# Kernel optimization log

Measured on AMD Instinct MI355X. Metric: run time of the kernel, lower is better.

## Reference

```python
import jax, jax.numpy as jnp
import numpy as np

HIDDEN = 1024
FFN = 2048
N_EXPERTS = 8
TOP_K = 2


def setup_inputs() -> dict:
    key = jax.random.key(0)
    k_x, k_g, k1, k2, k3 = jax.random.split(key, 5)
    hidden_states = jax.random.normal(k_x, (4, 4096, HIDDEN), dtype=jnp.float32)
    gate_w = jax.random.normal(k_g, (N_EXPERTS, HIDDEN), dtype=jnp.float32) * 0.02
    # nn.Linear convention: weight is [out_features, in_features]
    w1 = jax.random.normal(k1, (N_EXPERTS, FFN, HIDDEN), dtype=jnp.float32) * 0.02
    w2 = jax.random.normal(k2, (N_EXPERTS, HIDDEN, FFN), dtype=jnp.float32) * 0.02
    w3 = jax.random.normal(k3, (N_EXPERTS, FFN, HIDDEN), dtype=jnp.float32) * 0.02
    return {"hidden_states": hidden_states, "gate_w": gate_w, "w1": w1, "w2": w2, "w3": w3}


def reference(hidden_states, gate_w, w1, w2, w3):
    B, S, H = hidden_states.shape
    E = gate_w.shape[0]
    x = hidden_states.reshape(-1, H)  # [T, H]
    T = x.shape[0]

    # Router: softmax in fp32, top-2, renormalize (matches torch reference)
    router_logits = jnp.einsum("th,eh->te", x, gate_w)
    probs = jax.nn.softmax(router_logits.astype(jnp.float32), axis=-1)
    top_w, top_i = jax.lax.top_k(probs, TOP_K)  # [T, 2]
    top_w = top_w / jnp.sum(top_w, axis=-1, keepdims=True)
    top_w = top_w.astype(x.dtype)

    # Dense combine weights [T, E]: zero for unselected experts.
    combine = jnp.zeros((T, E), dtype=x.dtype)
    combine = combine.at[jnp.arange(T)[:, None], top_i].set(top_w)

    # Per-expert SwiGLU; loop over small fixed expert count, accumulate.
    out = jnp.zeros_like(x)
    for e in range(E):
        h = jax.nn.silu(x @ w1[e].T) * (x @ w3[e].T)  # [T, FFN]
        out = out + combine[:, e:e + 1] * (h @ w2[e].T)
    return out.reshape(B, S, H)
```

## Files before the change

### kernel.cpp

```cpp
#include <hip/hip_runtime.h>
#include <cstdint>

#define H 1024
#define F 2048
#define E_N 8
#define BM 128
#define BK 64

typedef __attribute__((ext_vector_type(8))) short short8v;
typedef __attribute__((ext_vector_type(4))) float float4v;
typedef unsigned short u16;

__device__ __forceinline__ u16 f2bf(float f) {
    uint32_t u = __float_as_uint(f);
    u += 0x7FFFu + ((u >> 16) & 1u);
    return (u16)(u >> 16);
}
__device__ __forceinline__ float bf2f(u16 b) {
    return __uint_as_float(((uint32_t)b) << 16);
}

__device__ __forceinline__ void gload16(const void* g, void* l) {
    __builtin_amdgcn_global_load_lds((const __attribute__((address_space(1))) uint32_t*)g,
                                     (__attribute__((address_space(3))) uint32_t*)l, 16, 0, 0);
}

__device__ __forceinline__ void decode_swz(int bid, int nTiles, int ngy, int gyc,
                                           int& tile, int& gy) {
    int nblk = nTiles * ngy;
    int q = nblk >> 3, r = nblk & 7;
    int xcd = bid & 7, pos = bid >> 3;
    int cid = (xcd < r ? xcd * (q + 1) : r * (q + 1) + (xcd - r) * q) + pos;
    int per = nTiles * gyc;
    int chunk = cid / per, rem = cid - chunk * per;
    tile = rem / gyc;
    gy = chunk * gyc + (rem - (rem / gyc) * gyc);
}

__global__ __launch_bounds__(256) void cvt_kernel(const float* __restrict__ src,
                                                  u16* __restrict__ dst, int n) {
    int i = (blockIdx.x * 256 + threadIdx.x) * 4;
    int stride = gridDim.x * 256 * 4;
    for (; i < n; i += stride) {
        float4 v = *(const float4*)(src + i);
        ushort4 o;
        o.x = f2bf(v.x); o.y = f2bf(v.y); o.z = f2bf(v.z); o.w = f2bf(v.w);
        *(ushort4*)(dst + i) = o;
    }
}

__global__ __launch_bounds__(256) void router_kernel(const float* __restrict__ x,
                                                     const float* __restrict__ gw,
                                                     int* __restrict__ topi,
                                                     float* __restrict__ topw, int T) {
    int wave = threadIdx.x >> 6, lane = threadIdx.x & 63;
    int t = blockIdx.x * 4 + wave;
    if (t >= T) return;
    const float4* xr = (const float4*)(x + (size_t)t * H);
    float4 xv[4];
#pragma unroll
    for (int i = 0; i < 4; i++) xv[i] = xr[i * 64 + lane];
    float acc[E_N];
#pragma unroll
    for (int e = 0; e < E_N; e++) {
        const float4* gr = (const float4*)(gw + e * H);
        float s = 0.f;
#pragma unroll
        for (int i = 0; i < 4; i++) {
            float4 g = gr[i * 64 + lane];
            s += xv[i].x * g.x + xv[i].y * g.y + xv[i].z * g.z + xv[i].w * g.w;
        }
        acc[e] = s;
    }
#pragma unroll
    for (int e = 0; e < E_N; e++) {
#pragma unroll
        for (int off = 32; off; off >>= 1) acc[e] += __shfl_xor(acc[e], off, 64);
    }
    if (lane == 0) {
        int i0 = 0;
#pragma unroll
        for (int e = 1; e < E_N; e++) if (acc[e] > acc[i0]) i0 = e;
        int i1 = -1;
#pragma unroll
        for (int e = 0; e < E_N; e++) {
            if (e == i0) continue;
            if (i1 < 0 || acc[e] > acc[i1]) i1 = e;
        }
        float e1 = __expf(acc[i1] - acc[i0]);
        float w0 = 1.f / (1.f + e1);
        float w1v = e1 / (1.f + e1);
        topi[t * 2] = i0; topi[t * 2 + 1] = i1;
        topw[t * 2] = w0; topw[t * 2 + 1] = w1v;
    }
}

__global__ __launch_bounds__(256) void hist_kernel(const int* __restrict__ topi,
                                                   int* __restrict__ counts, int n) {
    __shared__ int hc[E_N];
    if (threadIdx.x < E_N) hc[threadIdx.x] = 0;
    __syncthreads();
    for (int i = blockIdx.x * 256 + threadIdx.x; i < n; i += gridDim.x * 256)
        atomicAdd(&hc[topi[i]], 1);
    __syncthreads();
    if (threadIdx.x < E_N) atomicAdd(&counts[threadIdx.x], hc[threadIdx.x]);
}

__global__ void scan_kernel(const int* __restrict__ counts, int* __restrict__ offsets,
                            int* __restrict__ cursors, int* __restrict__ tileOff) {
    if (threadIdx.x == 0 && blockIdx.x == 0) {
        int o = 0, to = 0;
        for (int e = 0; e < E_N; e++) {
            offsets[e] = o; cursors[e] = o; tileOff[e] = to;
            o += counts[e];
            to += (counts[e] + BM - 1) / BM;
        }
        offsets[E_N] = o; tileOff[E_N] = to;
    }
}

__global__ __launch_bounds__(1024) void scatter_kernel(const int* __restrict__ topi,
                                                       const float* __restrict__ topw,
                                                       int* __restrict__ cursors,
                                                       int* __restrict__ perm_tok,
                                                       float* __restrict__ perm_gate,
                                                       int* __restrict__ inv, int n) {
    __shared__ int hc[E_N];
    __shared__ int base[E_N];
    int tid = threadIdx.x;
    if (tid < E_N) hc[tid] = 0;
    __syncthreads();
    int i = blockIdx.x * 1024 + tid;
    int e = 0, lrank = 0;
    bool ok = (i < n);
    if (ok) {
        e = topi[i];
        lrank = atomicAdd(&hc[e], 1);
    }
    __syncthreads();
    if (tid < E_N) base[tid] = atomicAdd(&cursors[tid], hc[tid]);
    __syncthreads();
    if (ok) {
        int pos = base[e] + lrank;
        perm_tok[pos] = i >> 1;
        perm_gate[pos] = topw[i];
        inv[i] = pos;
    }
}

__global__ __launch_bounds__(256) void stage1_kernel(
    const u16* __restrict__ xg, const u16* __restrict__ w1b, const u16* __restrict__ w3b,
    const int* __restrict__ perm_tok, const float* __restrict__ perm_gate,
    const int* __restrict__ offsets, const int* __restrict__ tileOff,
    u16* __restrict__ h, int cstart, int tpcThis) {
    __shared__ u16 lA[BM * BK];
    __shared__ u16 lB1[64 * BK];
    __shared__ u16 lB3[64 * BK];
    __shared__ int ptokS[BM];
    __shared__ float pgateS[BM];

    int tileL, nbIdx;
    decode_swz(blockIdx.x, tpcThis, F / 64, 4, tileL, nbIdx);
    int tile = cstart + tileL;
    if (tile >= tileOff[E_N]) return;
    int e = 0;
    while (e < E_N - 1 && tile >= tileOff[e + 1]) e++;
    int rbase = offsets[e] + (tile - tileOff[e]) * BM;
    int segEnd = offsets[e + 1];
    int e0 = 0;
    while (e0 < E_N - 1 && cstart >= tileOff[e0 + 1]) e0++;
    int chunkBase = offsets[e0] + (cstart - tileOff[e0]) * BM;

    int tid = threadIdx.x;
    if (tid < BM) {
        int p = rbase + tid; if (p > segEnd - 1) p = segEnd - 1;
        ptokS[tid] = perm_tok[p];
        pgateS[tid] = perm_gate[p];
    }
    __syncthreads();

    int lane = tid & 63, wave = tid >> 6;
    int mBase = (wave >> 1) * 64, nBaseW = (wave & 1) * 32;
    int lrow = lane & 15, kgrp = lane >> 4;
    int nb = nbIdx * 64;
    const u16* w1p = w1b + (size_t)e * F * H + (size_t)nb * H;
    const u16* w3p = w3b + (size_t)e * F * H + (size_t)nb * H;

    int lr = lane >> 3;
    int csw = ((lane & 7) ^ lr) << 3;

    const u16* aSrc[4];
#pragma unroll
    for (int j = 0; j < 4; j++) {
        int rb = (j * 4 + wave) * 8;
        int tok = ptokS[rb + lr];
        aSrc[j] = xg + (size_t)tok * H + csw;
    }
    const u16 *b1Src[2], *b3Src[2];
#pragma unroll
    for (int j = 0; j < 2; j++) {
        int rr = (j * 4 + wave) * 8 + lr;
        b1Src[j] = w1p + (size_t)rr * H + csw;
        b3Src[j] = w3p + (size_t)rr * H + csw;
    }

    float4v acc1[4][2], acc3[4][2];
#pragma unroll
    for (int a = 0; a < 4; a++)
#pragma unroll
        for (int b = 0; b < 2; b++) { acc1[a][b] = (float4v)(0.f); acc3[a][b] = (float4v)(0.f); }

    for (int kt = 0; kt < H / BK; kt++) {
        int ko = kt * BK;
#pragma unroll
        for (int j = 0; j < 4; j++)
            gload16(aSrc[j] + ko, &lA[((j * 4 + wave) * 8) * BK]);
#pragma unroll
        for (int j = 0; j < 2; j++) {
            int rb = (j * 4 + wave) * 8;
            gload16(b1Src[j] + ko, &lB1[rb * BK]);
            gload16(b3Src[j] + ko, &lB3[rb * BK]);
        }
        __syncthreads();
#pragma unroll
        for (int kk = 0; kk < 2; kk++) {
            int kg = kk * 4 + kgrp;
            short8v aF[4], b1F[2], b3F[2];
#pragma unroll
            for (int fm = 0; fm < 4; fm++) {
                int r = mBase + fm * 16 + lrow;
                aF[fm] = *(const short8v*)&lA[r * BK + ((kg ^ (r & 7)) << 3)];
            }
#pragma unroll
            for (int fn = 0; fn < 2; fn++) {
                int c = nBaseW + fn * 16 + lrow;
                b1F[fn] = *(const short8v*)&lB1[c * BK + ((kg ^ (c & 7)) << 3)];
                b3F[fn] = *(const short8v*)&lB3[c * BK + ((kg ^ (c & 7)) << 3)];
            }
#pragma unroll
            for (int fm = 0; fm < 4; fm++)
#pragma unroll
                for (int fn = 0; fn < 2; fn++) {
                    acc1[fm][fn] = __builtin_amdgcn_mfma_f32_16x16x32_bf16(aF[fm], b1F[fn], acc1[fm][fn], 0, 0, 0);
                    acc3[fm][fn] = __builtin_amdgcn_mfma_f32_16x16x32_bf16(aF[fm], b3F[fn], acc3[fm][fn], 0, 0, 0);
                }
        }
        __syncthreads();
    }
    int rif = (lane >> 4) * 4;
#pragma unroll
    for (int fm = 0; fm < 4; fm++) {
#pragma unroll
        for (int reg = 0; reg < 4; reg++) {
            int rowIdx = mBase + fm * 16 + rif + reg;
            int p = rbase + rowIdx;
            if (p < segEnd) {
                float g = pgateS[rowIdx];
#pragma unroll
                for (int fn = 0; fn < 2; fn++) {
                    float a1 = acc1[fm][fn][reg], a3 = acc3[fm][fn][reg];
                    float sv = a1 / (1.f + __expf(-a1));
                    float hv = sv * a3 * g;
                    int ncol = nb + nBaseW + fn * 16 + (lane & 15);
                    h[(size_t)(p - chunkBase) * F + ncol] = f2bf(hv);
                }
            }
        }
    }
}

__global__ __launch_bounds__(256) void stage2_kernel(
    const u16* __restrict__ h, const u16* __restrict__ w2b,
    const int* __restrict__ offsets, const int* __restrict__ tileOff,
    u16* __restrict__ y, int cstart, int tpcThis) {
    __shared__ u16 lA[BM * BK];
    __shared__ u16 lB[BM * BK];

    int tileL, nbIdx;
    decode_swz(blockIdx.x, tpcThis, H / 128, 4, tileL, nbIdx);
    int tile = cstart + tileL;
    if (tile >= tileOff[E_N]) return;
    int e = 0;
    while (e < E_N - 1 && tile >= tileOff[e + 1]) e++;
    int rbase = offsets[e] + (tile - tileOff[e]) * BM;
    int segEnd = offsets[e + 1];
    int e0 = 0;
    while (e0 < E_N - 1 && cstart >= tileOff[e0 + 1]) e0++;
    int chunkBase = offsets[e0] + (cstart - tileOff[e0]) * BM;

    int tid = threadIdx.x;
    int lane = tid & 63, wave = tid >> 6;
    int mBase = (wave >> 1) * 64, nBaseW = (wave & 1) * 64;
    int lrow = lane & 15, kgrp = lane >> 4;
    int nb = nbIdx * 128;
    const u16* w2p = w2b + (size_t)e * H * F + (size_t)nb * F;

    int lr = lane >> 3;
    int csw = ((lane & 7) ^ lr) << 3;

    const u16 *aSrc[4], *bSrc[4];
#pragma unroll
    for (int j = 0; j < 4; j++) {
        int rb = (j * 4 + wave) * 8;
        int p = rbase + rb + lr; if (p > segEnd - 1) p = segEnd - 1;
        aSrc[j] = h + (size_t)(p - chunkBase) * F + csw;
        int rr = rb + lr;
        bSrc[j] = w2p + (size_t)rr * F + csw;
    }

    float4v acc[4][4];
#pragma unroll
    for (int a = 0; a < 4; a++)
#pragma unroll
        for (int b = 0; b < 4; b++) acc[a][b] = (float4v)(0.f);

    for (int kt = 0; kt < F / BK; kt++) {
        int ko = kt * BK;
#pragma unroll
        for (int j = 0; j < 4; j++) {
            int rb = (j * 4 + wave) * 8;
            gload16(aSrc[j] + ko, &lA[rb * BK]);
            gload16(bSrc[j] + ko, &lB[rb * BK]);
        }
        __syncthreads();
#pragma unroll
        for (int kk = 0; kk < 2; kk++) {
            int kg = kk * 4 + kgrp;
            short8v aF[4], bF[4];
#pragma unroll
            for (int fm = 0; fm < 4; fm++) {
                int r = mBase + fm * 16 + lrow;
                aF[fm] = *(const short8v*)&lA[r * BK + ((kg ^ (r & 7)) << 3)];
            }
#pragma unroll
            for (int fn = 0; fn < 4; fn++) {
                int c = nBaseW + fn * 16 + lrow;
                bF[fn] = *(const short8v*)&lB[c * BK + ((kg ^ (c & 7)) << 3)];
            }
#pragma unroll
            for (int fm = 0; fm < 4; fm++)
#pragma unroll
                for (int fn = 0; fn < 4; fn++)
                    acc[fm][fn] = __builtin_amdgcn_mfma_f32_16x16x32_bf16(aF[fm], bF[fn], acc[fm][fn], 0, 0, 0);
        }
        __syncthreads();
    }
    int rif = (lane >> 4) * 4;
#pragma unroll
    for (int fm = 0; fm < 4; fm++) {
#pragma unroll
        for (int reg = 0; reg < 4; reg++) {
            int rowIdx = mBase + fm * 16 + rif + reg;
            int p = rbase + rowIdx;
            if (p < segEnd) {
#pragma unroll
                for (int fn = 0; fn < 4; fn++) {
                    int n = nb + nBaseW + fn * 16 + (lane & 15);
                    y[(size_t)p * H + n] = f2bf(acc[fm][fn][reg]);
                }
            }
        }
    }
}

__global__ __launch_bounds__(256) void combine_kernel(const u16* __restrict__ y,
                                                      const int* __restrict__ inv,
                                                      float* __restrict__ out) {
    int t = blockIdx.x, c = threadIdx.x;
    int s0 = inv[t * 2], s1 = inv[t * 2 + 1];
    ushort4 a = *(const ushort4*)(y + (size_t)s0 * H + c * 4);
    ushort4 b = *(const ushort4*)(y + (size_t)s1 * H + c * 4);
    float4 o;
    o.x = bf2f(a.x) + bf2f(b.x);
    o.y = bf2f(a.y) + bf2f(b.y);
    o.z = bf2f(a.z) + bf2f(b.z);
    o.w = bf2f(a.w) + bf2f(b.w);
    *(float4*)(out + (size_t)t * H + c * 4) = o;
}

extern "C" void kernel_launch(void* const* d_in, const int* in_sizes, int n_in,
                              void* d_out, int out_size, void* d_ws, size_t ws_size,
                              hipStream_t stream) {
    (void)n_in; (void)out_size;
    const float* x  = (const float*)d_in[0];
    const float* gw = (const float*)d_in[1];
    const float* w1 = (const float*)d_in[2];
    const float* w2 = (const float*)d_in[3];
    const float* w3 = (const float*)d_in[4];
    float* out = (float*)d_out;
    int T = in_sizes[0] / H;
    int P = T * 2;

    char* ws = (char*)d_ws;
    size_t off = 0;
    auto alloc = [&](size_t b) { size_t c = off; off = (off + b + 255) & ~(size_t)255; return c; };
    size_t misc_o  = alloc(256);
    int* counts  = (int*)(ws + misc_o);
    int* offsets = (int*)(ws + misc_o + 64);
    int* cursors = (int*)(ws + misc_o + 128);
    int* tileOff = (int*)(ws + misc_o + 192);
    size_t topi_o  = alloc((size_t)T * 2 * 4);
    size_t topw_o  = alloc((size_t)T * 2 * 4);
    size_t ptok_o  = alloc((size_t)P * 4);
    size_t pgate_o = alloc((size_t)P * 4);
    size_t inv_o   = alloc((size_t)T * 2 * 4);
    size_t w1b_o = alloc((size_t)E_N * F * H * 2);
    size_t w3b_o = alloc((size_t)E_N * F * H * 2);
    size_t w2b_o = alloc((size_t)E_N * H * F * 2);
    size_t xg_o  = alloc((size_t)T * H * 2);
    size_t y_o   = alloc((size_t)P * H * 2);

    int maxTiles = P / BM + E_N;
    size_t perTile = (size_t)BM * F * 2;
    size_t avail = (ws_size > off + 256) ? (ws_size - off - 256) : 0;
    int tpc = (int)(avail / perTile);
    if (tpc > maxTiles) tpc = maxTiles;
    if (tpc < 8) tpc = 8;
    size_t h_o = alloc((size_t)tpc * perTile);

    hipMemsetAsync(ws + misc_o, 0, 256, stream);

    int nW = E_N * F * H;
    cvt_kernel<<<4096, 256, 0, stream>>>(w1, (u16*)(ws + w1b_o), nW);
    cvt_kernel<<<4096, 256, 0, stream>>>(w3, (u16*)(ws + w3b_o), nW);
    cvt_kernel<<<4096, 256, 0, stream>>>(w2, (u16*)(ws + w2b_o), nW);
    cvt_kernel<<<4096, 256, 0, stream>>>(x,  (u16*)(ws + xg_o),  T * H);

    router_kernel<<<T / 4, 256, 0, stream>>>(x, gw, (int*)(ws + topi_o), (float*)(ws + topw_o), T);
    hist_kernel<<<32, 256, 0, stream>>>((int*)(ws + topi_o), counts, P);
    scan_kernel<<<1, 64, 0, stream>>>(counts, offsets, cursors, tileOff);
    scatter_kernel<<<(P + 1023) / 1024, 1024, 0, stream>>>(
        (int*)(ws + topi_o), (float*)(ws + topw_o), cursors,
        (int*)(ws + ptok_o), (float*)(ws + pgate_o), (int*)(ws + inv_o), P);

    for (int cstart = 0; cstart < maxTiles; cstart += tpc) {
        int tpcThis = maxTiles - cstart; if (tpcThis > tpc) tpcThis = tpc;
        stage1_kernel<<<tpcThis * (F / 64), 256, 0, stream>>>(
            (u16*)(ws + xg_o), (u16*)(ws + w1b_o), (u16*)(ws + w3b_o),
            (int*)(ws + ptok_o), (float*)(ws + pgate_o), offsets, tileOff,
            (u16*)(ws + h_o), cstart, tpcThis);
        stage2_kernel<<<tpcThis * (H / 128), 256, 0, stream>>>(
            (u16*)(ws + h_o), (u16*)(ws + w2b_o), offsets, tileOff,
            (u16*)(ws + y_o), cstart, tpcThis);
    }
    combine_kernel<<<T, 256, 0, stream>>>((u16*)(ws + y_o), (int*)(ws + inv_o), out);
}
```

Measured before the change: 752.6 us.

## Double-buffer LDS tiles in both expert GEMM stages to overlap loads with MFMA

Both grouped-GEMM kernels now use two LDS buffers per operand and prefetch the next K-tile with global_load_lds while MFMAs run on the current tile. An explicit vmcnt(0) wait plus one barrier per iteration replaces the old load-then-sync-then-compute pattern. The aim is to hide global memory latency behind compute. In exchange, LDS use per block doubles, which may reduce occupancy.

```diff
diff --git a/kernel.cpp b/kernel.cpp
--- a/kernel.cpp
+++ b/kernel.cpp
@@ -153,9 +153,9 @@
     const int* __restrict__ perm_tok, const float* __restrict__ perm_gate,
     const int* __restrict__ offsets, const int* __restrict__ tileOff,
     u16* __restrict__ h, int cstart, int tpcThis) {
-    __shared__ u16 lA[BM * BK];
-    __shared__ u16 lB1[64 * BK];
-    __shared__ u16 lB3[64 * BK];
+    __shared__ u16 lA[2][BM * BK];
+    __shared__ u16 lB1[2][64 * BK];
+    __shared__ u16 lB3[2][64 * BK];
     __shared__ int ptokS[BM];
     __shared__ float pgateS[BM];
 
@@ -204,24 +204,32 @@
         b3Src[j] = w3p + (size_t)rr * H + csw;
     }
 
-    float4v acc1[4][2], acc3[4][2];
-#pragma unroll
-    for (int a = 0; a < 4; a++)
-#pragma unroll
-        for (int b = 0; b < 2; b++) { acc1[a][b] = (float4v)(0.f); acc3[a][b] = (float4v)(0.f); }
-
-    for (int kt = 0; kt < H / BK; kt++) {
+    auto stage = [&](int kt, int b) {
         int ko = kt * BK;
 #pragma unroll
         for (int j = 0; j < 4; j++)
-            gload16(aSrc[j] + ko, &lA[((j * 4 + wave) * 8) * BK]);
+            gload16(aSrc[j] + ko, &lA[b][((j * 4 + wave) * 8) * BK]);
 #pragma unroll
         for (int j = 0; j < 2; j++) {
             int rb = (j * 4 + wave) * 8;
-            gload16(b1Src[j] + ko, &lB1[rb * BK]);
-            gload16(b3Src[j] + ko, &lB3[rb * BK]);
-        }
-        __syncthreads();
+            gload16(b1Src[j] + ko, &lB1[b][rb * BK]);
+            gload16(b3Src[j] + ko, &lB3[b][rb * BK]);
+        }
+    };
+
+    float4v acc1[4][2], acc3[4][2];
+#pragma unroll
+    for (int a = 0; a < 4; a++)
+#pragma unroll
+        for (int b = 0; b < 2; b++) { acc1[a][b] = (float4v)(0.f); acc3[a][b] = (float4v)(0.f); }
+
+    stage(0, 0);
+    asm volatile("s_waitcnt vmcnt(0)" ::: "memory");
+    __syncthreads();
+
+    for (int kt = 0; kt < H / BK; kt++) {
+        int cur = kt & 1;
+        if (kt + 1 < H / BK) stage(kt + 1, cur ^ 1);
 #pragma unroll
         for (int kk = 0; kk < 2; kk++) {
             int kg = kk * 4 + kgrp;
@@ -229,13 +237,13 @@
 #pragma unroll
             for (int fm = 0; fm < 4; fm++) {
                 int r = mBase + fm * 16 + lrow;
-                aF[fm] = *(const short8v*)&lA[r * BK + ((kg ^ (r & 7)) << 3)];
+                aF[fm] = *(const short8v*)&lA[cur][r * BK + ((kg ^ (r & 7)) << 3)];
             }
 #pragma unroll
             for (int fn = 0; fn < 2; fn++) {
                 int c = nBaseW + fn * 16 + lrow;
-                b1F[fn] = *(const short8v*)&lB1[c * BK + ((kg ^ (c & 7)) << 3)];
-                b3F[fn] = *(const short8v*)&lB3[c * BK + ((kg ^ (c & 7)) << 3)];
+                b1F[fn] = *(const short8v*)&lB1[cur][c * BK + ((kg ^ (c & 7)) << 3)];
+                b3F[fn] = *(const short8v*)&lB3[cur][c * BK + ((kg ^ (c & 7)) << 3)];
             }
 #pragma unroll
             for (int fm = 0; fm < 4; fm++)
@@ -245,6 +253,7 @@
                     acc3[fm][fn] = __builtin_amdgcn_mfma_f32_16x16x32_bf16(aF[fm], b3F[fn], acc3[fm][fn], 0, 0, 0);
                 }
         }
+        asm volatile("s_waitcnt vmcnt(0)" ::: "memory");
         __syncthreads();
     }
     int rif = (lane >> 4) * 4;
@@ -273,8 +282,8 @@
     const u16* __restrict__ h, const u16* __restrict__ w2b,
     const int* __restrict__ offsets, const int* __restrict__ tileOff,
     u16* __restrict__ y, int cstart, int tpcThis) {
-    __shared__ u16 lA[BM * BK];
-    __shared__ u16 lB[BM * BK];
+    __shared__ u16 lA[2][BM * BK];
+    __shared__ u16 lB[2][BM * BK];
 
     int tileL, nbIdx;
     decode_swz(blockIdx.x, tpcThis, H / 128, 4, tileL, nbIdx);
@@ -308,21 +317,29 @@
         bSrc[j] = w2p + (size_t)rr * F + csw;
     }
 
-    float4v acc[4][4];
-#pragma unroll
-    for (int a = 0; a < 4; a++)
-#pragma unroll
-        for (int b = 0; b < 4; b++) acc[a][b] = (float4v)(0.f);
-
-    for (int kt = 0; kt < F / BK; kt++) {
+    auto stage = [&](int kt, int b) {
         int ko = kt * BK;
 #pragma unroll
         for (int j = 0; j < 4; j++) {
             int rb = (j * 4 + wave) * 8;
-            gload16(aSrc[j] + ko, &lA[rb * BK]);
-            gload16(bSrc[j] + ko, &lB[rb * BK]);
-        }
-        __syncthreads();
+            gload16(aSrc[j] + ko, &lA[b][rb * BK]);
+            gload16(bSrc[j] + ko, &lB[b][rb * BK]);
+        }
+    };
+
+    float4v acc[4][4];
+#pragma unroll
+    for (int a = 0; a < 4; a++)
+#pragma unroll
+        for (int b = 0; b < 4; b++) acc[a][b] = (float4v)(0.f);
+
+    stage(0, 0);
+    asm volatile("s_waitcnt vmcnt(0)" ::: "memory");
+    __syncthreads();
+
+    for (int kt = 0; kt < F / BK; kt++) {
+        int cur = kt & 1;
+        if (kt + 1 < F / BK) stage(kt + 1, cur ^ 1);
 #pragma unroll
         for (int kk = 0; kk < 2; kk++) {
             int kg = kk * 4 + kgrp;
@@ -330,12 +347,12 @@
 #pragma unroll
             for (int fm = 0; fm < 4; fm++) {
                 int r = mBase + fm * 16 + lrow;
-                aF[fm] = *(const short8v*)&lA[r * BK + ((kg ^ (r & 7)) << 3)];
+                aF[fm] = *(const short8v*)&lA[cur][r * BK + ((kg ^ (r & 7)) << 3)];
             }
 #pragma unroll
             for (int fn = 0; fn < 4; fn++) {
                 int c = nBaseW + fn * 16 + lrow;
-                bF[fn] = *(const short8v*)&lB[c * BK + ((kg ^ (c & 7)) << 3)];
+                bF[fn] = *(const short8v*)&lB[cur][c * BK + ((kg ^ (c & 7)) << 3)];
             }
 #pragma unroll
             for (int fm = 0; fm < 4; fm++)
@@ -343,6 +360,7 @@
                 for (int fn = 0; fn < 4; fn++)
                     acc[fm][fn] = __builtin_amdgcn_mfma_f32_16x16x32_bf16(aF[fm], bF[fn], acc[fm][fn], 0, 0, 0);
         }
+        asm volatile("s_waitcnt vmcnt(0)" ::: "memory");
         __syncthreads();
     }
     int rif = (lane >> 4) * 4;
```

Measured after the change: 829.8 us. 1.1x slower.

## Double-buffer expert GEMMs with 256-row tiles and interleaved prefetch

Applied to the files above, without the earlier changes.

Both expert GEMM stages now use 256-row tiles with 512-thread blocks and double-buffered LDS. The next K-slice's global-to-LDS loads are interleaved with MFMA phases under explicit vmcnt waits, barriers and setprio. This is meant to hide memory latency and raise arithmetic intensity per block. Stage 2 picks a 256- or 128-wide N tile depending on how many tiles a chunk has. In exchange it uses more registers and LDS per block and wastes more work on partially filled expert tiles.

```diff
diff --git a/kernel.cpp b/kernel.cpp
--- a/kernel.cpp
+++ b/kernel.cpp
@@ -4,7 +4,7 @@
 #define H 1024
 #define F 2048
 #define E_N 8
-#define BM 128
+#define BM 256
 #define BK 64
 
 typedef __attribute__((ext_vector_type(8))) short short8v;
@@ -23,6 +23,12 @@
 __device__ __forceinline__ void gload16(const void* g, void* l) {
     __builtin_amdgcn_global_load_lds((const __attribute__((address_space(1))) uint32_t*)g,
                                      (__attribute__((address_space(3))) uint32_t*)l, 16, 0, 0);
+}
+
+__device__ __forceinline__ void barx() {
+    asm volatile("" ::: "memory");
+    __builtin_amdgcn_s_barrier();
+    asm volatile("" ::: "memory");
 }
 
 __device__ __forceinline__ void decode_swz(int bid, int nTiles, int ngy, int gyc,
@@ -148,19 +154,19 @@
     }
 }
 
-__global__ __launch_bounds__(256) void stage1_kernel(
+__global__ __launch_bounds__(512) void stage1_kernel(
     const u16* __restrict__ xg, const u16* __restrict__ w1b, const u16* __restrict__ w3b,
     const int* __restrict__ perm_tok, const float* __restrict__ perm_gate,
     const int* __restrict__ offsets, const int* __restrict__ tileOff,
     u16* __restrict__ h, int cstart, int tpcThis) {
-    __shared__ u16 lA[BM * BK];
-    __shared__ u16 lB1[64 * BK];
-    __shared__ u16 lB3[64 * BK];
+    __shared__ u16 lA[2][BM * BK];
+    __shared__ u16 lB1[2][128 * BK];
+    __shared__ u16 lB3[2][128 * BK];
     __shared__ int ptokS[BM];
     __shared__ float pgateS[BM];
 
     int tileL, nbIdx;
-    decode_swz(blockIdx.x, tpcThis, F / 64, 4, tileL, nbIdx);
+    decode_swz(blockIdx.x, tpcThis, F / 128, 4, tileL, nbIdx);
     int tile = cstart + tileL;
     if (tile >= tileOff[E_N]) return;
     int e = 0;
@@ -179,89 +185,122 @@
     }
     __syncthreads();
 
-    int lane = tid & 63, wave = tid >> 6;
-    int mBase = (wave >> 1) * 64, nBaseW = (wave & 1) * 32;
+    int lane = tid & 63, wid = tid >> 6;
+    int wr = wid >> 2, wc = wid & 3;
     int lrow = lane & 15, kgrp = lane >> 4;
-    int nb = nbIdx * 64;
+    int lr = lane >> 3, csw = ((lane & 7) ^ lr) << 3;
+    int nb = nbIdx * 128;
     const u16* w1p = w1b + (size_t)e * F * H + (size_t)nb * H;
     const u16* w3p = w3b + (size_t)e * F * H + (size_t)nb * H;
 
-    int lr = lane >> 3;
-    int csw = ((lane & 7) ^ lr) << 3;
-
-    const u16* aSrc[4];
+    int aOff[4];
 #pragma unroll
     for (int j = 0; j < 4; j++) {
-        int rb = (j * 4 + wave) * 8;
-        int tok = ptokS[rb + lr];
-        aSrc[j] = xg + (size_t)tok * H + csw;
-    }
-    const u16 *b1Src[2], *b3Src[2];
-#pragma unroll
-    for (int j = 0; j < 2; j++) {
-        int rr = (j * 4 + wave) * 8 + lr;
-        b1Src[j] = w1p + (size_t)rr * H + csw;
-        b3Src[j] = w3p + (size_t)rr * H + csw;
-    }
-
-    float4v acc1[4][2], acc3[4][2];
-#pragma unroll
-    for (int a = 0; a < 4; a++)
+        int rb = (j * 8 + wid) * 8;
+        aOff[j] = ptokS[rb + lr] * H + csw;
+    }
+    int bOff[2];
+#pragma unroll
+    for (int j = 0; j < 2; j++) bOff[j] = ((j * 8 + wid) * 8 + lr) * H + csw;
+
+    auto stA  = [&](int cc, int ko, int j) { gload16(xg  + aOff[j] + ko, &lA[cc][(j * 8 + wid) * 8 * BK]); };
+    auto stB1 = [&](int cc, int ko, int j) { gload16(w1p + bOff[j] + ko, &lB1[cc][(j * 8 + wid) * 8 * BK]); };
+    auto stB3 = [&](int cc, int ko, int j) { gload16(w3p + bOff[j] + ko, &lB3[cc][(j * 8 + wid) * 8 * BK]); };
+
+    float4v acc1[8][2], acc3[8][2];
+#pragma unroll
+    for (int a = 0; a < 8; a++)
 #pragma unroll
         for (int b = 0; b < 2; b++) { acc1[a][b] = (float4v)(0.f); acc3[a][b] = (float4v)(0.f); }
 
-    for (int kt = 0; kt < H / BK; kt++) {
-        int ko = kt * BK;
-#pragma unroll
-        for (int j = 0; j < 4; j++)
-            gload16(aSrc[j] + ko, &lA[((j * 4 + wave) * 8) * BK]);
-#pragma unroll
-        for (int j = 0; j < 2; j++) {
-            int rb = (j * 4 + wave) * 8;
-            gload16(b1Src[j] + ko, &lB1[rb * BK]);
-            gload16(b3Src[j] + ko, &lB3[rb * BK]);
-        }
-        __syncthreads();
-#pragma unroll
-        for (int kk = 0; kk < 2; kk++) {
-            int kg = kk * 4 + kgrp;
-            short8v aF[4], b1F[2], b3F[2];
-#pragma unroll
-            for (int fm = 0; fm < 4; fm++) {
-                int r = mBase + fm * 16 + lrow;
-                aF[fm] = *(const short8v*)&lA[r * BK + ((kg ^ (r & 7)) << 3)];
+    stB1(0, 0, 0); stB1(0, 0, 1);
+    stB3(0, 0, 0); stB3(0, 0, 1);
+    stA(0, 0, 0);  stA(0, 0, 2);
+    stA(0, 0, 1);  stA(0, 0, 3);
+    asm volatile("s_waitcnt vmcnt(2)" ::: "memory");
+    barx();
+
+#define S1_DS(p) \
+    short8v aF##p[2][2]; \
+    _Pragma("unroll") \
+    for (int pm = 0; pm < 2; pm++) { \
+        int r = wr * 128 + (2 * p + pm) * 16 + lrow; \
+        _Pragma("unroll") \
+        for (int kk = 0; kk < 2; kk++) \
+            aF##p[pm][kk] = *(const short8v*)&Ac[r * BK + (((kk * 4 + kgrp) ^ (r & 7)) << 3)]; \
+    }
+#define S1_MM(p) \
+    __builtin_amdgcn_s_setprio(1); \
+    _Pragma("unroll") \
+    for (int pm = 0; pm < 2; pm++) \
+    _Pragma("unroll") \
+    for (int n = 0; n < 2; n++) \
+    _Pragma("unroll") \
+    for (int kk = 0; kk < 2; kk++) { \
+        acc1[2 * p + pm][n] = __builtin_amdgcn_mfma_f32_16x16x32_bf16(aF##p[pm][kk], b1F[n][kk], acc1[2 * p + pm][n], 0, 0, 0); \
+        acc3[2 * p + pm][n] = __builtin_amdgcn_mfma_f32_16x16x32_bf16(aF##p[pm][kk], b3F[n][kk], acc3[2 * p + pm][n], 0, 0, 0); \
+    } \
+    __builtin_amdgcn_s_setprio(0);
+
+    const int NT = H / BK;
+    for (int t = 0; t < NT; t++) {
+        int c = t & 1, cN = c ^ 1;
+        int ko = (t + 1) * BK;
+        bool pf = (t + 1 < NT);
+        const u16* Ac = lA[c]; const u16* B1c = lB1[c]; const u16* B3c = lB3[c];
+        short8v b1F[2][2], b3F[2][2];
+#pragma unroll
+        for (int n = 0; n < 2; n++) {
+            int col = wc * 32 + n * 16 + lrow;
+#pragma unroll
+            for (int kk = 0; kk < 2; kk++) {
+                int so = col * BK + (((kk * 4 + kgrp) ^ (col & 7)) << 3);
+                b1F[n][kk] = *(const short8v*)&B1c[so];
+                b3F[n][kk] = *(const short8v*)&B3c[so];
             }
-#pragma unroll
-            for (int fn = 0; fn < 2; fn++) {
-                int c = nBaseW + fn * 16 + lrow;
-                b1F[fn] = *(const short8v*)&lB1[c * BK + ((kg ^ (c & 7)) << 3)];
-                b3F[fn] = *(const short8v*)&lB3[c * BK + ((kg ^ (c & 7)) << 3)];
-            }
-#pragma unroll
-            for (int fm = 0; fm < 4; fm++)
-#pragma unroll
-                for (int fn = 0; fn < 2; fn++) {
-                    acc1[fm][fn] = __builtin_amdgcn_mfma_f32_16x16x32_bf16(aF[fm], b1F[fn], acc1[fm][fn], 0, 0, 0);
-                    acc3[fm][fn] = __builtin_amdgcn_mfma_f32_16x16x32_bf16(aF[fm], b3F[fn], acc3[fm][fn], 0, 0, 0);
-                }
-        }
-        __syncthreads();
-    }
+        }
+        S1_DS(0)
+        if (pf) { stB1(cN, ko, 0); stB1(cN, ko, 1); }
+        barx();
+        S1_MM(0)
+        barx();
+        S1_DS(1)
+        if (pf) { stB3(cN, ko, 0); stB3(cN, ko, 1); }
+        barx();
+        S1_MM(1)
+        if (pf) asm volatile("s_waitcnt vmcnt(4)" ::: "memory");
+        else    asm volatile("s_waitcnt vmcnt(0)" ::: "memory");
+        barx();
+        S1_DS(2)
+        if (pf) { stA(cN, ko, 0); stA(cN, ko, 2); }
+        barx();
+        S1_MM(2)
+        barx();
+        S1_DS(3)
+        if (pf) { stA(cN, ko, 1); stA(cN, ko, 3); }
+        barx();
+        S1_MM(3)
+        asm volatile("s_waitcnt vmcnt(2)" ::: "memory");
+        barx();
+    }
+#undef S1_DS
+#undef S1_MM
+
     int rif = (lane >> 4) * 4;
 #pragma unroll
-    for (int fm = 0; fm < 4; fm++) {
+    for (int m = 0; m < 8; m++) {
 #pragma unroll
         for (int reg = 0; reg < 4; reg++) {
-            int rowIdx = mBase + fm * 16 + rif + reg;
+            int rowIdx = wr * 128 + m * 16 + rif + reg;
             int p = rbase + rowIdx;
             if (p < segEnd) {
                 float g = pgateS[rowIdx];
 #pragma unroll
-                for (int fn = 0; fn < 2; fn++) {
-                    float a1 = acc1[fm][fn][reg], a3 = acc3[fm][fn][reg];
+                for (int n = 0; n < 2; n++) {
+                    float a1 = acc1[m][n][reg], a3 = acc3[m][n][reg];
                     float sv = a1 / (1.f + __expf(-a1));
                     float hv = sv * a3 * g;
-                    int ncol = nb + nBaseW + fn * 16 + (lane & 15);
+                    int ncol = nb + wc * 32 + n * 16 + (lane & 15);
                     h[(size_t)(p - chunkBase) * F + ncol] = f2bf(hv);
                 }
             }
@@ -269,15 +308,17 @@
     }
 }
 
-__global__ __launch_bounds__(256) void stage2_kernel(
+template<int NREP>
+__global__ __launch_bounds__(512) void stage2_kernel(
     const u16* __restrict__ h, const u16* __restrict__ w2b,
     const int* __restrict__ offsets, const int* __restrict__ tileOff,
     u16* __restrict__ y, int cstart, int tpcThis) {
-    __shared__ u16 lA[BM * BK];
-    __shared__ u16 lB[BM * BK];
+    constexpr int BN = NREP * 64;
+    __shared__ u16 lA[2][BM * BK];
+    __shared__ u16 lB[2][BN * BK];
 
     int tileL, nbIdx;
-    decode_swz(blockIdx.x, tpcThis, H / 128, 4, tileL, nbIdx);
+    decode_swz(blockIdx.x, tpcThis, H / BN, 4, tileL, nbIdx);
     int tile = cstart + tileL;
     if (tile >= tileOff[E_N]) return;
     int e = 0;
@@ -289,74 +330,120 @@
     int chunkBase = offsets[e0] + (cstart - tileOff[e0]) * BM;
 
     int tid = threadIdx.x;
-    int lane = tid & 63, wave = tid >> 6;
-    int mBase = (wave >> 1) * 64, nBaseW = (wave & 1) * 64;
+    int lane = tid & 63, wid = tid >> 6;
+    int wr = wid >> 2, wc = wid & 3;
     int lrow = lane & 15, kgrp = lane >> 4;
-    int nb = nbIdx * 128;
+    int lr = lane >> 3, csw = ((lane & 7) ^ lr) << 3;
+    int nb = nbIdx * BN;
     const u16* w2p = w2b + (size_t)e * H * F + (size_t)nb * F;
 
-    int lr = lane >> 3;
-    int csw = ((lane & 7) ^ lr) << 3;
-
-    const u16 *aSrc[4], *bSrc[4];
+    int aOff[4];
 #pragma unroll
     for (int j = 0; j < 4; j++) {
-        int rb = (j * 4 + wave) * 8;
+        int rb = (j * 8 + wid) * 8;
         int p = rbase + rb + lr; if (p > segEnd - 1) p = segEnd - 1;
-        aSrc[j] = h + (size_t)(p - chunkBase) * F + csw;
-        int rr = rb + lr;
-        bSrc[j] = w2p + (size_t)rr * F + csw;
-    }
-
-    float4v acc[4][4];
-#pragma unroll
-    for (int a = 0; a < 4; a++)
-#pragma unroll
-        for (int b = 0; b < 4; b++) acc[a][b] = (float4v)(0.f);
-
-    for (int kt = 0; kt < F / BK; kt++) {
-        int ko = kt * BK;
-#pragma unroll
-        for (int j = 0; j < 4; j++) {
-            int rb = (j * 4 + wave) * 8;
-            gload16(aSrc[j] + ko, &lA[rb * BK]);
-            gload16(bSrc[j] + ko, &lB[rb * BK]);
-        }
-        __syncthreads();
-#pragma unroll
-        for (int kk = 0; kk < 2; kk++) {
-            int kg = kk * 4 + kgrp;
-            short8v aF[4], bF[4];
-#pragma unroll
-            for (int fm = 0; fm < 4; fm++) {
-                int r = mBase + fm * 16 + lrow;
-                aF[fm] = *(const short8v*)&lA[r * BK + ((kg ^ (r & 7)) << 3)];
-            }
-#pragma unroll
-            for (int fn = 0; fn < 4; fn++) {
-                int c = nBaseW + fn * 16 + lrow;
-                bF[fn] = *(const short8v*)&lB[c * BK + ((kg ^ (c & 7)) << 3)];
-            }
-#pragma unroll
-            for (int fm = 0; fm < 4; fm++)
-#pragma unroll
-                for (int fn = 0; fn < 4; fn++)
-                    acc[fm][fn] = __builtin_amdgcn_mfma_f32_16x16x32_bf16(aF[fm], bF[fn], acc[fm][fn], 0, 0, 0);
-        }
-        __syncthreads();
-    }
+        aOff[j] = (p - chunkBase) * F + csw;
+    }
+    int bOff[NREP];
+#pragma unroll
+    for (int j = 0; j < NREP; j++) bOff[j] = ((j * 8 + wid) * 8 + lr) * F + csw;
+
+    auto stA = [&](int cc, int ko, int j) { gload16(h   + aOff[j] + ko, &lA[cc][(j * 8 + wid) * 8 * BK]); };
+    auto stB = [&](int cc, int ko, int j) { gload16(w2p + bOff[j] + ko, &lB[cc][(j * 8 + wid) * 8 * BK]); };
+
+    float4v acc[8][NREP];
+#pragma unroll
+    for (int a = 0; a < 8; a++)
+#pragma unroll
+        for (int b = 0; b < NREP; b++) acc[a][b] = (float4v)(0.f);
+
+#pragma unroll
+    for (int j = 0; j < NREP; j++) stB(0, 0, j);
+    stA(0, 0, 0); stA(0, 0, 2);
+    stA(0, 0, 1); stA(0, 0, 3);
+    asm volatile("s_waitcnt vmcnt(2)" ::: "memory");
+    barx();
+
+#define S2_DS(p) \
+    short8v aF##p[2][2]; \
+    _Pragma("unroll") \
+    for (int pm = 0; pm < 2; pm++) { \
+        int r = wr * 128 + (2 * p + pm) * 16 + lrow; \
+        _Pragma("unroll") \
+        for (int kk = 0; kk < 2; kk++) \
+            aF##p[pm][kk] = *(const short8v*)&Ac[r * BK + (((kk * 4 + kgrp) ^ (r & 7)) << 3)]; \
+    }
+#define S2_MM(p) \
+    __builtin_amdgcn_s_setprio(1); \
+    _Pragma("unroll") \
+    for (int pm = 0; pm < 2; pm++) \
+    _Pragma("unroll") \
+    for (int n = 0; n < NREP; n++) \
+    _Pragma("unroll") \
+    for (int kk = 0; kk < 2; kk++) \
+        acc[2 * p + pm][n] = __builtin_amdgcn_mfma_f32_16x16x32_bf16(aF##p[pm][kk], bF[n][kk], acc[2 * p + pm][n], 0, 0, 0); \
+    __builtin_amdgcn_s_setprio(0);
+
+    const int NT = F / BK;
+    for (int t = 0; t < NT; t++) {
+        int c = t & 1, cN = c ^ 1;
+        int ko = (t + 1) * BK;
+        bool pf = (t + 1 < NT);
+        const u16* Ac = lA[c]; const u16* Bc = lB[c];
+        short8v bF[NREP][2];
+#pragma unroll
+        for (int n = 0; n < NREP; n++) {
+            int col = wc * (BN / 4) + n * 16 + lrow;
+#pragma unroll
+            for (int kk = 0; kk < 2; kk++)
+                bF[n][kk] = *(const short8v*)&Bc[col * BK + (((kk * 4 + kgrp) ^ (col & 7)) << 3)];
+        }
+        S2_DS(0)
+        if (pf) { stB(cN, ko, 0); if constexpr (NREP == 4) stB(cN, ko, 1); }
+        barx();
+        S2_MM(0)
+        barx();
+        S2_DS(1)
+        if (pf) {
+            if constexpr (NREP == 4) { stB(cN, ko, 2); stB(cN, ko, 3); }
+            else stB(cN, ko, 1);
+        }
+        barx();
+        S2_MM(1)
+        if (pf) {
+            if constexpr (NREP == 4) asm volatile("s_waitcnt vmcnt(4)" ::: "memory");
+            else                     asm volatile("s_waitcnt vmcnt(2)" ::: "memory");
+        } else {
+            asm volatile("s_waitcnt vmcnt(0)" ::: "memory");
+        }
+        barx();
+        S2_DS(2)
+        if (pf) { stA(cN, ko, 0); stA(cN, ko, 2); }
+        barx();
+        S2_MM(2)
+        barx();
+        S2_DS(3)
+        if (pf) { stA(cN, ko, 1); stA(cN, ko, 3); }
+        barx();
+        S2_MM(3)
+        asm volatile("s_waitcnt vmcnt(2)" ::: "memory");
+        barx();
+    }
+#undef S2_DS
+#undef S2_MM
+
     int rif = (lane >> 4) * 4;
 #pragma unroll
-    for (int fm = 0; fm < 4; fm++) {
+    for (int m = 0; m < 8; m++) {
 #pragma unroll
         for (int reg = 0; reg < 4; reg++) {
-            int rowIdx = mBase + fm * 16 + rif + reg;
+            int rowIdx = wr * 128 + m * 16 + rif + reg;
             int p = rbase + rowIdx;
             if (p < segEnd) {
 #pragma unroll
-                for (int fn = 0; fn < 4; fn++) {
-                    int n = nb + nBaseW + fn * 16 + (lane & 15);
-                    y[(size_t)p * H + n] = f2bf(acc[fm][fn][reg]);
+                for (int n = 0; n < NREP; n++) {
+                    int col = nb + wc * (BN / 4) + n * 16 + (lane & 15);
+                    y[(size_t)p * H + col] = f2bf(acc[m][n][reg]);
                 }
             }
         }
@@ -415,7 +502,7 @@
     size_t avail = (ws_size > off + 256) ? (ws_size - off - 256) : 0;
     int tpc = (int)(avail / perTile);
     if (tpc > maxTiles) tpc = maxTiles;
-    if (tpc < 8) tpc = 8;
+    if (tpc < 4) tpc = 4;
     size_t h_o = alloc((size_t)tpc * perTile);
 
     hipMemsetAsync(ws + misc_o, 0, 256, stream);
@@ -435,13 +522,18 @@
 
     for (int cstart = 0; cstart < maxTiles; cstart += tpc) {
         int tpcThis = maxTiles - cstart; if (tpcThis > tpc) tpcThis = tpc;
-        stage1_kernel<<<tpcThis * (F / 64), 256, 0, stream>>>(
+        stage1_kernel<<<tpcThis * (F / 128), 512, 0, stream>>>(
             (u16*)(ws + xg_o), (u16*)(ws + w1b_o), (u16*)(ws + w3b_o),
             (int*)(ws + ptok_o), (float*)(ws + pgate_o), offsets, tileOff,
             (u16*)(ws + h_o), cstart, tpcThis);
-        stage2_kernel<<<tpcThis * (H / 128), 256, 0, stream>>>(
-            (u16*)(ws + h_o), (u16*)(ws + w2b_o), offsets, tileOff,
-            (u16*)(ws + y_o), cstart, tpcThis);
+        if (tpcThis >= 54)
+            stage2_kernel<4><<<tpcThis * (H / 256), 512, 0, stream>>>(
+                (u16*)(ws + h_o), (u16*)(ws + w2b_o), offsets, tileOff,
+                (u16*)(ws + y_o), cstart, tpcThis);
+        else
+            stage2_kernel<2><<<tpcThis * (H / 128), 512, 0, stream>>>(
+                (u16*)(ws + h_o), (u16*)(ws + w2b_o), offsets, tileOff,
+                (u16*)(ws + y_o), cstart, tpcThis);
     }
     combine_kernel<<<T, 256, 0, stream>>>((u16*)(ws + y_o), (int*)(ws + inv_o), out);
 }
```

After: 688.8 us. 8.5% less time.
